# Kernel tuning notes

Hardware: AMD Instinct MI355X
Metric: run time of the kernel (lower is better)

## Reference

```python
import jax, jax.numpy as jnp
import numpy as np

NEG_SLOPE = 0.2  # PyG GATConv default negative_slope
N_NODES = 50000


def gat_conv(x, src, dst, W, att_src, att_dst, bias, heads, out_ch):
    # x: [N, F_in]; src/dst: [E] (messages flow src -> dst, softmax over dst)
    N = x.shape[0]
    h = (x @ W).reshape(N, heads, out_ch)              # [N,H,C]
    a_src = jnp.sum(h * att_src, axis=-1)              # [N,H]
    a_dst = jnp.sum(h * att_dst, axis=-1)              # [N,H]
    e = jax.nn.leaky_relu(a_src[src] + a_dst[dst], NEG_SLOPE)   # [E,H]
    # numerically stable segment softmax over incoming edges of each dst node
    m = jax.ops.segment_max(e, dst, num_segments=N)    # [N,H]
    e = jnp.exp(e - m[dst])
    denom = jax.ops.segment_sum(e, dst, num_segments=N)
    alpha = e / (denom[dst] + 1e-16)                   # [E,H]
    msg = h[src] * alpha[:, :, None]                   # [E,H,C]
    out = jax.ops.segment_sum(msg, dst, num_segments=N)  # [N,H,C]
    return out.reshape(N, heads * out_ch) + bias


def add_self_loops(edge_index, num_nodes):
    loop = jnp.arange(num_nodes, dtype=edge_index.dtype)
    return jnp.concatenate([edge_index, jnp.stack([loop, loop])], axis=1)


def setup_inputs() -> dict:
    key = jax.random.key(0)
    ks = jax.random.split(key, 10)
    F_in, H, C, F_out = 256, 4, 64, 16
    x = jax.random.normal(ks[0], (N_NODES, F_in), dtype=jnp.float32)
    edge_index = jax.random.randint(ks[1], (2, 800000), 0, N_NODES, dtype=jnp.int64)
    s1 = 1.0 / np.sqrt(F_in)
    s2 = 1.0 / np.sqrt(H * C)
    return {
        "x": x,
        "edge_index": edge_index,
        "W1": jax.random.normal(ks[2], (F_in, H * C), dtype=jnp.float32) * s1,
        "att_src1": jax.random.normal(ks[3], (H, C), dtype=jnp.float32) * s2,
        "att_dst1": jax.random.normal(ks[4], (H, C), dtype=jnp.float32) * s2,
        "b1": jnp.zeros((H * C,), dtype=jnp.float32),
        "W2": jax.random.normal(ks[5], (H * C, F_out), dtype=jnp.float32) * s2,
        "att_src2": jax.random.normal(ks[6], (1, F_out), dtype=jnp.float32) * 0.25,
        "att_dst2": jax.random.normal(ks[7], (1, F_out), dtype=jnp.float32) * 0.25,
        "b2": jnp.zeros((F_out,), dtype=jnp.float32),
    }


def reference(x, edge_index, W1, att_src1, att_dst1, b1, W2, att_src2, att_dst2, b2):
    ei = add_self_loops(edge_index, x.shape[0])
    src, dst = ei[0], ei[1]
    H1, C1 = att_src1.shape
    h = gat_conv(x, src, dst, W1, att_src1, att_dst1, b1, H1, C1)
    h = jax.nn.relu(h)
    # F.dropout(training=False) is identity in eval mode
    H2, C2 = att_src2.shape
    out = gat_conv(h, src, dst, W2, att_src2, att_dst2, b2, H2, C2)
    return jax.nn.log_softmax(out, axis=1)
```

## Files before the change

kernel.cpp:

```cpp
#include <hip/hip_runtime.h>
#include <math.h>


typedef __attribute__((ext_vector_type(8))) short bf16x8;
typedef __attribute__((ext_vector_type(8))) unsigned short u16x8;
typedef __attribute__((ext_vector_type(4))) float f32x4;
typedef __attribute__((ext_vector_type(2))) float f32x2;

static __device__ inline unsigned short f2bf(float f) {
    unsigned u = __builtin_bit_cast(unsigned, f);
    unsigned r = (u + 0x7FFF + ((u >> 16) & 1)) >> 16;
    return (unsigned short)r;
}
static __device__ inline float bf2f(unsigned short u) {
    unsigned v = ((unsigned)u) << 16;
    return __builtin_bit_cast(float, v);
}
static __device__ inline float lrelu(float x) { return x > 0.f ? x : 0.2f * x; }

__global__ __launch_bounds__(256) void k_prep(const float* __restrict__ x,
                                              const float* __restrict__ W1,
                                              const float* __restrict__ b1,
                                              const float* __restrict__ W2,
                                              short* __restrict__ xb,
                                              int* __restrict__ csr,
                                              short* __restrict__ w1t,
                                              float* __restrict__ b1p,
                                              float* __restrict__ w2p,
                                              int* __restrict__ cnt,
                                              float* __restrict__ a1s,
                                              float* __restrict__ a2s,
                                              unsigned* __restrict__ h1f8u,
                                              float* __restrict__ h2,
                                              int N) {
    long idx = (long)blockIdx.x * 256 + threadIdx.x;
    const long T = (long)N * 32;
    if (idx < T) {
        const float* xp = x + idx * 8;
        float4 f0 = *(const float4*)xp;
        float4 f1 = *(const float4*)(xp + 4);
        short b[8];
        b[0] = (short)f2bf(f0.x); b[1] = (short)f2bf(f0.y);
        b[2] = (short)f2bf(f0.z); b[3] = (short)f2bf(f0.w);
        b[4] = (short)f2bf(f1.x); b[5] = (short)f2bf(f1.y);
        b[6] = (short)f2bf(f1.z); b[7] = (short)f2bf(f1.w);
        *(bf16x8*)(xb + idx * 8) = *(bf16x8*)&b[0];
        long p = idx * 2;
        int v0 = ((p & 63) == 0) ? (int)((p >> 6) << 4) : (N << 4);
        int v1 = N << 4;
        *(int2*)(csr + p) = make_int2(v0, v1);
    }
    if (idx < N) cnt[idx] = 1;
    if (idx < 256) {
        int ct = ((int)idx >> 6) * 64 + ((int)idx & 3) * 16 + (((int)idx & 63) >> 2);
        b1p[idx] = b1[ct];
    }
    if (idx < 4096) {
        int pp = (int)idx >> 4, c2 = (int)idx & 15;
        int ct = (pp >> 6) * 64 + (pp & 3) * 16 + ((pp & 63) >> 2);
        w2p[idx] = W2[ct * 16 + c2];
    }
    if (idx < 4) a1s[(long)N * 4 + idx] = -1e30f;
    if (idx == 4) a2s[N] = -1e30f;
    if (idx < 64) h1f8u[(long)N * 64 + idx] = 0u;
    if (idx < 16) h2[(long)N * 16 + idx] = 0.f;
    if (idx < 65536) {
        int n = (int)idx >> 8, k = (int)idx & 255;
        w1t[n * 256 + k] = (short)f2bf(W1[k * 256 + n]);
    }
}

__global__ __launch_bounds__(256) void k_scatter(const int* __restrict__ ei,
                                                 int* __restrict__ cnt,
                                                 int* __restrict__ csr,
                                                 int E0) {
    int e0 = (blockIdx.x * 256 + threadIdx.x) << 2;
    if (e0 >= E0) return;
    if (e0 + 4 <= E0) {
        int4 s4 = *(const int4*)&ei[e0];
        int4 d4 = *(const int4*)&ei[E0 + e0];
        int ss[4] = {s4.x, s4.y, s4.z, s4.w};
        int dd[4] = {d4.x, d4.y, d4.z, d4.w};
        int sl[4];
#pragma unroll
        for (int q = 0; q < 4; ++q) sl[q] = atomicAdd(&cnt[dd[q]], 1);
#pragma unroll
        for (int q = 0; q < 4; ++q)
            if (sl[q] < 64) csr[((long)dd[q] << 6) + sl[q]] = ss[q] << 4;
    } else {
        for (int e = e0; e < E0; ++e) {
            int s = ei[e], d = ei[E0 + e];
            int slot = atomicAdd(&cnt[d], 1);
            if (slot < 64) csr[((long)d << 6) + slot] = s << 4;
        }
    }
}

__global__ __launch_bounds__(256) void k_gemm1_mfma(const short* __restrict__ Ab,
                                                    const short* __restrict__ Bt,
                                                    const float* __restrict__ att_s,
                                                    const float* __restrict__ att_d,
                                                    unsigned char* __restrict__ C8,
                                                    float* __restrict__ a1s,
                                                    float* __restrict__ a1d,
                                                    int M) {
    __shared__ short As[64][40];
    __shared__ short Bs[128][40];
    const int bm = blockIdx.y * 64;
    const int bn = blockIdx.x * 128;
    const int tid = threadIdx.x;
    const int lane = tid & 63;
    const int wave = tid >> 6;
    const int wm = (wave >> 1) * 32;
    const int wn = (wave & 1) * 64;
    const int l15 = lane & 15;
    const int l4 = lane >> 4;

    const int ar = tid >> 2, aq = (tid & 3) * 8;
    const int br = tid >> 1, bh = (tid & 1) * 16;

    f32x4 acc[2][4] = {};

    for (int k0 = 0; k0 < 256; k0 += 32) {
        {
            bf16x8 av;
            if (bm + ar < M) {
                av = *(const bf16x8*)&Ab[(long)(bm + ar) * 256 + k0 + aq];
            } else {
#pragma unroll
                for (int q = 0; q < 8; ++q) av[q] = 0;
            }
            *(bf16x8*)&As[ar][aq] = av;
            const short* p = &Bt[(long)(bn + br) * 256 + k0 + bh];
            *(bf16x8*)&Bs[br][bh] = *(const bf16x8*)p;
            *(bf16x8*)&Bs[br][bh + 8] = *(const bf16x8*)(p + 8);
        }
        __syncthreads();

        bf16x8 af[2], bfr[4];
#pragma unroll
        for (int i = 0; i < 2; ++i)
            af[i] = *(const bf16x8*)&As[wm + i * 16 + l15][l4 * 8];
#pragma unroll
        for (int j = 0; j < 4; ++j)
            bfr[j] = *(const bf16x8*)&Bs[wn + j * 16 + l15][l4 * 8];
#pragma unroll
        for (int i = 0; i < 2; ++i)
#pragma unroll
            for (int j = 0; j < 4; ++j)
                acc[i][j] = __builtin_amdgcn_mfma_f32_16x16x32_bf16(af[i], bfr[j], acc[i][j], 0, 0, 0);
        __syncthreads();
    }

    const int h = (bn + wn) >> 6;
    float aws[4], awd[4];
#pragma unroll
    for (int j = 0; j < 4; ++j) {
        aws[j] = att_s[h * 64 + j * 16 + l15];
        awd[j] = att_d[h * 64 + j * 16 + l15];
    }

#pragma unroll
    for (int i = 0; i < 2; ++i) {
#pragma unroll
        for (int r = 0; r < 4; ++r) {
            float sv = 0.f, dv = 0.f;
#pragma unroll
            for (int j = 0; j < 4; ++j) {
                sv += acc[i][j][r] * aws[j];
                dv += acc[i][j][r] * awd[j];
            }
#pragma unroll
            for (int o = 1; o < 16; o <<= 1) {
                sv += __shfl_xor(sv, o);
                dv += __shfl_xor(dv, o);
            }
            int row = bm + wm + i * 16 + l4 * 4 + r;
            if (row < M) {
                if (l15 == 0) { a1s[row * 4 + h] = sv; a1d[row * 4 + h] = dv; }
                int d = 0;
                d = __builtin_amdgcn_cvt_pk_fp8_f32(acc[i][0][r], acc[i][1][r], d, false);
                d = __builtin_amdgcn_cvt_pk_fp8_f32(acc[i][2][r], acc[i][3][r], d, true);
                *(unsigned*)&C8[(long)row * 256 + (bn + wn) + l15 * 4] = (unsigned)d;
            }
        }
    }
}

__global__ __launch_bounds__(256) void k_gather1(const unsigned char* __restrict__ h1f8,
                                                 const int* __restrict__ cnt,
                                                 const int* __restrict__ csr,
                                                 const float* __restrict__ as1,
                                                 const float* __restrict__ ad1,
                                                 const float* __restrict__ b1p,
                                                 unsigned short* __restrict__ out1b,
                                                 int N) {
    int wid = blockIdx.x * 4 + (threadIdx.x >> 6);
    int lane = threadIdx.x & 63;
    if (wid >= N) return;

    const int es = lane >> 4;
    const int cl = lane & 15;
    const int hc = cl >> 2;
    const float adh = ad1[wid * 4 + hc];

    int c = min(cnt[wid], 64);
    int len4 = (c + 3) & ~3;
    const int* seg = csr + ((long)wid << 6);
    const char* as1c = (const char*)as1 + hc * 4;
    const char* h1c  = (const char*)h1f8 + cl * 16;

    float dacc = 0.f;
    f32x2 acc2[8] = {};
#pragma unroll 2
    for (int j0 = 0; j0 < len4; j0 += 4) {
        int sv = seg[j0 + es];
        float a = __expf(lrelu(*(const float*)(as1c + sv) + adh));
        dacc += a;
        f32x2 av = {a, a};
        uint4 v = *(const uint4*)(h1c + ((long)sv << 4));
        unsigned w[4] = {v.x, v.y, v.z, v.w};
#pragma unroll
        for (int q = 0; q < 4; ++q) {
            f32x2 lo = __builtin_amdgcn_cvt_pk_f32_fp8((int)w[q], false);
            f32x2 hi = __builtin_amdgcn_cvt_pk_f32_fp8((int)w[q], true);
            acc2[q * 2 + 0] += av * lo;
            acc2[q * 2 + 1] += av * hi;
        }
    }
    dacc += __shfl_xor(dacc, 16);
    dacc += __shfl_xor(dacc, 32);
    const float inv_c = 1.f / (dacc + 1e-16f);

    float accf[16];
#pragma unroll
    for (int q = 0; q < 8; ++q) { accf[2 * q] = acc2[q].x; accf[2 * q + 1] = acc2[q].y; }
#pragma unroll
    for (int q = 0; q < 16; ++q) {
        accf[q] += __shfl_xor(accf[q], 16);
        accf[q] += __shfl_xor(accf[q], 32);
    }
    if (lane < 16) {
        unsigned pk[8];
#pragma unroll
        for (int q = 0; q < 8; ++q) {
            float v0 = fmaxf(accf[q * 2 + 0] * inv_c + b1p[cl * 16 + q * 2 + 0], 0.f);
            float v1 = fmaxf(accf[q * 2 + 1] * inv_c + b1p[cl * 16 + q * 2 + 1], 0.f);
            pk[q] = (unsigned)f2bf(v0) | ((unsigned)f2bf(v1) << 16);
        }
        unsigned short* dst = &out1b[(long)wid * 256 + cl * 16];
        *(uint4*)dst = make_uint4(pk[0], pk[1], pk[2], pk[3]);
        *(uint4*)(dst + 8) = make_uint4(pk[4], pk[5], pk[6], pk[7]);
    }
}

__global__ __launch_bounds__(256) void k_gemm2(const unsigned short* __restrict__ Xb,
                                               const float* __restrict__ Wp,
                                               const float* __restrict__ att_s,
                                               const float* __restrict__ att_d,
                                               float* __restrict__ h2,
                                               float* __restrict__ a2s,
                                               float* __restrict__ a2d, int N) {
    __shared__ float Ws[256 * 16];
    for (int i = threadIdx.x; i < 1024; i += 256)
        ((float4*)Ws)[i] = ((const float4*)Wp)[i];
    __syncthreads();
    int r = threadIdx.x >> 4, c = threadIdx.x & 15;
    int row = blockIdx.x * 16 + r;
    if (row >= N) return;
    const unsigned short* xr = Xb + (long)row * 256;
    float acc = 0.f;
    for (int k = 0; k < 256; k += 8) {
        u16x8 xv = *(const u16x8*)&xr[k];
#pragma unroll
        for (int q = 0; q < 8; ++q)
            acc += bf2f(xv[q]) * Ws[(k + q) * 16 + c];
    }
    h2[row * 16 + c] = acc;
    float vs = acc * att_s[c];
    float vd = acc * att_d[c];
    for (int o = 1; o < 16; o <<= 1) { vs += __shfl_xor(vs, o); vd += __shfl_xor(vd, o); }
    if (c == 0) { a2s[row] = vs; a2d[row] = vd; }
}

__global__ __launch_bounds__(256) void k_gather2(const float* __restrict__ h2,
                                                 const int* __restrict__ cnt,
                                                 const int* __restrict__ csr,
                                                 const float* __restrict__ a2s,
                                                 const float* __restrict__ a2d,
                                                 const float* __restrict__ b2,
                                                 float* __restrict__ out, int N) {
    int wid = blockIdx.x * 4 + (threadIdx.x >> 6);
    int lane = threadIdx.x & 63;
    if (wid >= N) return;
    float adh = a2d[wid];
    const int es = lane >> 4;
    const int c = lane & 15;

    int cc = min(cnt[wid], 64);
    int len4 = (cc + 3) & ~3;
    const int* seg = csr + ((long)wid << 6);
    const char* a2c = (const char*)a2s;
    const char* h2c = (const char*)h2 + c * 4;

    float dacc = 0.f;
    float acc = 0.f;
#pragma unroll 2
    for (int j0 = 0; j0 < len4; j0 += 4) {
        int sv = seg[j0 + es];
        float a = __expf(lrelu(*(const float*)(a2c + (sv >> 2)) + adh));
        dacc += a;
        acc += a * *(const float*)(h2c + (sv << 2));
    }
    acc += __shfl_xor(acc, 16);
    acc += __shfl_xor(acc, 32);
    dacc += __shfl_xor(dacc, 16);
    dacc += __shfl_xor(dacc, 32);
    float inv = 1.f / (dacc + 1e-16f);
    float v = acc * inv + b2[c];
    float mx = v;
    for (int o = 1; o < 16; o <<= 1) mx = fmaxf(mx, __shfl_xor(mx, o));
    float se = __expf(v - mx);
    for (int o = 1; o < 16; o <<= 1) se += __shfl_xor(se, o);
    float r = v - mx - logf(se);
    if (lane < 16) out[(long)wid * 16 + c] = r;
}

extern "C" void kernel_launch(void* const* d_in, const int* in_sizes, int n_in,
                              void* d_out, int out_size, void* d_ws, size_t ws_size,
                              hipStream_t stream) {
    const float* x    = (const float*)d_in[0];
    const int*   ei   = (const int*)d_in[1];
    const float* W1   = (const float*)d_in[2];
    const float* as1w = (const float*)d_in[3];
    const float* ad1w = (const float*)d_in[4];
    const float* b1   = (const float*)d_in[5];
    const float* W2   = (const float*)d_in[6];
    const float* as2w = (const float*)d_in[7];
    const float* ad2w = (const float*)d_in[8];
    const float* b2   = (const float*)d_in[9];
    float* out = (float*)d_out;

    const int N  = in_sizes[0] / 256;
    const int E0 = in_sizes[1] / 2;

    char* p = (char*)d_ws;
    unsigned char*  h1f8  = (unsigned char*)p;  p += (size_t)(N + 1) * 256;
    unsigned short* out1b = (unsigned short*)p; p += (size_t)N * 256 * sizeof(short);
    float* h2     = (float*)p; p += (size_t)(N + 1) * 16 * sizeof(float);
    float* a1s    = (float*)p; p += (size_t)(N + 1) * 4 * sizeof(float);
    float* a1d    = (float*)p; p += (size_t)N * 4 * sizeof(float);
    float* a2s    = (float*)p; p += (size_t)(N + 1) * sizeof(float);
    float* a2d    = (float*)p; p += (size_t)N * sizeof(float);
    float* b1p    = (float*)p; p += (size_t)256 * sizeof(float);
    float* w2p    = (float*)p; p += (size_t)4096 * sizeof(float);
    int*   cnt    = (int*)p;   p += (size_t)N * sizeof(int);
    short* w1t    = (short*)p; p += (size_t)256 * 256 * sizeof(short);
    int*   csr    = (int*)p;   p += (size_t)N * 64 * sizeof(int);

    short* xb = (short*)out1b;

    const int NW = (N + 3) / 4;

    const long T = (long)N * 32;
    hipLaunchKernelGGL(k_prep, dim3((unsigned)((T + 255) / 256)), dim3(256), 0, stream,
                       x, W1, b1, W2, xb, csr, w1t, b1p, w2p, cnt, a1s, a2s,
                       (unsigned*)h1f8, h2, N);

    const int E4 = (E0 + 3) / 4;
    hipLaunchKernelGGL(k_scatter, dim3((E4 + 255) / 256), dim3(256), 0, stream,
                       ei, cnt, csr, E0);

    hipLaunchKernelGGL(k_gemm1_mfma, dim3(2, (N + 63) / 64), dim3(256), 0, stream,
                       xb, w1t, as1w, ad1w, h1f8, a1s, a1d, N);
    hipLaunchKernelGGL(k_gather1, dim3(NW), dim3(256), 0, stream,
                       h1f8, cnt, csr, a1s, a1d, b1p, out1b, N);

    hipLaunchKernelGGL(k_gemm2, dim3((N + 15) / 16), dim3(256), 0, stream,
                       out1b, w2p, as2w, ad2w, h2, a2s, a2d, N);
    hipLaunchKernelGGL(k_gather2, dim3(NW), dim3(256), 0, stream,
                       h2, cnt, csr, a2s, a2d, b2, out, N);
}
```

Before: 263.8 us.

## Fuse layer-2 linear and attention projection into layer-1 gather epilogue

The layer-1 aggregation kernel now applies bias and ReLU, multiplies by W2 in registers, reduces across lanes, and writes h2 and the layer-2 attention scalars directly. This removes the bf16 round trip of the 50000x256 hidden activations and one kernel launch. The edge scatter kernel also handles 8 edges per thread instead of 4. In exchange the gather epilogue gains extra shuffles and W2 reads per node, and the hidden activations stay in fp32 rather than being rounded to bf16.

Measured after the change: 308.0 us. +16.7%, slower.

```diff
diff --git a/kernel.cpp b/kernel.cpp
--- a/kernel.cpp
+++ b/kernel.cpp
@@ -74,18 +74,20 @@
                                                  int* __restrict__ cnt,
                                                  int* __restrict__ csr,
                                                  int E0) {
-    int e0 = (blockIdx.x * 256 + threadIdx.x) << 2;
+    int e0 = (blockIdx.x * 256 + threadIdx.x) << 3;
     if (e0 >= E0) return;
-    if (e0 + 4 <= E0) {
-        int4 s4 = *(const int4*)&ei[e0];
-        int4 d4 = *(const int4*)&ei[E0 + e0];
-        int ss[4] = {s4.x, s4.y, s4.z, s4.w};
-        int dd[4] = {d4.x, d4.y, d4.z, d4.w};
-        int sl[4];
-#pragma unroll
-        for (int q = 0; q < 4; ++q) sl[q] = atomicAdd(&cnt[dd[q]], 1);
-#pragma unroll
-        for (int q = 0; q < 4; ++q)
+    if (e0 + 8 <= E0) {
+        int4 sa = *(const int4*)&ei[e0];
+        int4 sb = *(const int4*)&ei[e0 + 4];
+        int4 da = *(const int4*)&ei[E0 + e0];
+        int4 db = *(const int4*)&ei[E0 + e0 + 4];
+        int ss[8] = {sa.x, sa.y, sa.z, sa.w, sb.x, sb.y, sb.z, sb.w};
+        int dd[8] = {da.x, da.y, da.z, da.w, db.x, db.y, db.z, db.w};
+        int sl[8];
+#pragma unroll
+        for (int q = 0; q < 8; ++q) sl[q] = atomicAdd(&cnt[dd[q]], 1);
+#pragma unroll
+        for (int q = 0; q < 8; ++q)
             if (sl[q] < 64) csr[((long)dd[q] << 6) + sl[q]] = ss[q] << 4;
     } else {
         for (int e = e0; e < E0; ++e) {
@@ -187,14 +189,19 @@
     }
 }
 
-__global__ __launch_bounds__(256) void k_gather1(const unsigned char* __restrict__ h1f8,
-                                                 const int* __restrict__ cnt,
-                                                 const int* __restrict__ csr,
-                                                 const float* __restrict__ as1,
-                                                 const float* __restrict__ ad1,
-                                                 const float* __restrict__ b1p,
-                                                 unsigned short* __restrict__ out1b,
-                                                 int N) {
+__global__ __launch_bounds__(256) void k_gather1f(const unsigned char* __restrict__ h1f8,
+                                                  const int* __restrict__ cnt,
+                                                  const int* __restrict__ csr,
+                                                  const float* __restrict__ as1,
+                                                  const float* __restrict__ ad1,
+                                                  const float* __restrict__ b1p,
+                                                  const float* __restrict__ w2p,
+                                                  const float* __restrict__ as2w,
+                                                  const float* __restrict__ ad2w,
+                                                  float* __restrict__ h2,
+                                                  float* __restrict__ a2s,
+                                                  float* __restrict__ a2d,
+                                                  int N) {
     int wid = blockIdx.x * 4 + (threadIdx.x >> 6);
     int lane = threadIdx.x & 63;
     if (wid >= N) return;
@@ -240,47 +247,39 @@
         accf[q] += __shfl_xor(accf[q], 16);
         accf[q] += __shfl_xor(accf[q], 32);
     }
-    if (lane < 16) {
-        unsigned pk[8];
-#pragma unroll
-        for (int q = 0; q < 8; ++q) {
-            float v0 = fmaxf(accf[q * 2 + 0] * inv_c + b1p[cl * 16 + q * 2 + 0], 0.f);
-            float v1 = fmaxf(accf[q * 2 + 1] * inv_c + b1p[cl * 16 + q * 2 + 1], 0.f);
-            pk[q] = (unsigned)f2bf(v0) | ((unsigned)f2bf(v1) << 16);
-        }
-        unsigned short* dst = &out1b[(long)wid * 256 + cl * 16];
-        *(uint4*)dst = make_uint4(pk[0], pk[1], pk[2], pk[3]);
-        *(uint4*)(dst + 8) = make_uint4(pk[4], pk[5], pk[6], pk[7]);
-    }
-}
-
-__global__ __launch_bounds__(256) void k_gemm2(const unsigned short* __restrict__ Xb,
-                                               const float* __restrict__ Wp,
-                                               const float* __restrict__ att_s,
-                                               const float* __restrict__ att_d,
-                                               float* __restrict__ h2,
-                                               float* __restrict__ a2s,
-                                               float* __restrict__ a2d, int N) {
-    __shared__ float Ws[256 * 16];
-    for (int i = threadIdx.x; i < 1024; i += 256)
-        ((float4*)Ws)[i] = ((const float4*)Wp)[i];
-    __syncthreads();
-    int r = threadIdx.x >> 4, c = threadIdx.x & 15;
-    int row = blockIdx.x * 16 + r;
-    if (row >= N) return;
-    const unsigned short* xr = Xb + (long)row * 256;
-    float acc = 0.f;
-    for (int k = 0; k < 256; k += 8) {
-        u16x8 xv = *(const u16x8*)&xr[k];
-#pragma unroll
-        for (int q = 0; q < 8; ++q)
-            acc += bf2f(xv[q]) * Ws[(k + q) * 16 + c];
-    }
-    h2[row * 16 + c] = acc;
-    float vs = acc * att_s[c];
-    float vd = acc * att_d[c];
-    for (int o = 1; o < 16; o <<= 1) { vs += __shfl_xor(vs, o); vd += __shfl_xor(vd, o); }
-    if (c == 0) { a2s[row] = vs; a2d[row] = vd; }
+
+    float bv[16];
+    {
+        const float4* bp = (const float4*)(b1p + cl * 16);
+        *(float4*)&bv[0]  = bp[0];
+        *(float4*)&bv[4]  = bp[1];
+        *(float4*)&bv[8]  = bp[2];
+        *(float4*)&bv[12] = bp[3];
+    }
+    float val[16];
+#pragma unroll
+    for (int q = 0; q < 16; ++q) val[q] = fmaxf(accf[q] * inv_c + bv[q], 0.f);
+
+    float p0 = 0.f, p1 = 0.f, p2 = 0.f, p3 = 0.f;
+#pragma unroll
+    for (int q = 0; q < 16; ++q) {
+        float4 w = *(const float4*)&w2p[((cl * 16 + q) << 4) + (es << 2)];
+        p0 += val[q] * w.x; p1 += val[q] * w.y;
+        p2 += val[q] * w.z; p3 += val[q] * w.w;
+    }
+#pragma unroll
+    for (int o = 1; o < 16; o <<= 1) {
+        p0 += __shfl_xor(p0, o); p1 += __shfl_xor(p1, o);
+        p2 += __shfl_xor(p2, o); p3 += __shfl_xor(p3, o);
+    }
+    float4 asw = *(const float4*)(as2w + (es << 2));
+    float4 adw = *(const float4*)(ad2w + (es << 2));
+    float vs = p0 * asw.x + p1 * asw.y + p2 * asw.z + p3 * asw.w;
+    float vd = p0 * adw.x + p1 * adw.y + p2 * adw.z + p3 * adw.w;
+    vs += __shfl_xor(vs, 16); vs += __shfl_xor(vs, 32);
+    vd += __shfl_xor(vd, 16); vd += __shfl_xor(vd, 32);
+    if (lane == 0) { a2s[wid] = vs; a2d[wid] = vd; }
+    if (cl == 0) *(float4*)&h2[(long)wid * 16 + (es << 2)] = make_float4(p0, p1, p2, p3);
 }
 
 __global__ __launch_bounds__(256) void k_gather2(const float* __restrict__ h2,
@@ -346,7 +345,7 @@
 
     char* p = (char*)d_ws;
     unsigned char*  h1f8  = (unsigned char*)p;  p += (size_t)(N + 1) * 256;
-    unsigned short* out1b = (unsigned short*)p; p += (size_t)N * 256 * sizeof(short);
+    short* xb     = (short*)p; p += (size_t)N * 256 * sizeof(short);
     float* h2     = (float*)p; p += (size_t)(N + 1) * 16 * sizeof(float);
     float* a1s    = (float*)p; p += (size_t)(N + 1) * 4 * sizeof(float);
     float* a1d    = (float*)p; p += (size_t)N * 4 * sizeof(float);
@@ -358,8 +357,6 @@
     short* w1t    = (short*)p; p += (size_t)256 * 256 * sizeof(short);
     int*   csr    = (int*)p;   p += (size_t)N * 64 * sizeof(int);
 
-    short* xb = (short*)out1b;
-
     const int NW = (N + 3) / 4;
 
     const long T = (long)N * 32;
@@ -367,17 +364,17 @@
                        x, W1, b1, W2, xb, csr, w1t, b1p, w2p, cnt, a1s, a2s,
                        (unsigned*)h1f8, h2, N);
 
-    const int E4 = (E0 + 3) / 4;
-    hipLaunchKernelGGL(k_scatter, dim3((E4 + 255) / 256), dim3(256), 0, stream,
+    const int E8 = (E0 + 7) / 8;
+    hipLaunchKernelGGL(k_scatter, dim3((E8 + 255) / 256), dim3(256), 0, stream,
                        ei, cnt, csr, E0);
 
     hipLaunchKernelGGL(k_gemm1_mfma, dim3(2, (N + 63) / 64), dim3(256), 0, stream,
                        xb, w1t, as1w, ad1w, h1f8, a1s, a1d, N);
-    hipLaunchKernelGGL(k_gather1, dim3(NW), dim3(256), 0, stream,
-                       h1f8, cnt, csr, a1s, a1d, b1p, out1b, N);
-
-    hipLaunchKernelGGL(k_gemm2, dim3((N + 15) / 16), dim3(256), 0, stream,
-                       out1b, w2p, as2w, ad2w, h2, a2s, a2d, N);
+
+    hipLaunchKernelGGL(k_gather1f, dim3(NW), dim3(256), 0, stream,
+                       h1f8, cnt, csr, a1s, a1d, b1p, w2p, as2w, ad2w,
+                       h2, a2s, a2d, N);
+
     hipLaunchKernelGGL(k_gather2, dim3(NW), dim3(256), 0, stream,
                        h2, cnt, csr, a2s, a2d, b2, out, N);
 }
```
